# Kernel tuning notes

Measured on AMD Instinct MI355X. Metric: run time of the kernel, lower is better.

## Reference

```python
import jax, jax.numpy as jnp
import numpy as np

N, C, E, K = 50000, 128, 640000, 40  # nodes, feat dim, edges, classes
EPS = 1e-5


def setup_inputs() -> dict:
    key = jax.random.key(0)
    ks = jax.random.split(key, 8)
    s = 1.0 / np.sqrt(C)
    return {
        "x": jax.random.normal(ks[0], (N, C), jnp.float32),
        "edge_index": jax.random.randint(ks[1], (2, E), 0, N, dtype=jnp.int32),
        "W_conv": jax.random.normal(ks[2], (C, C), jnp.float32) * s,
        "b_conv": jnp.zeros((C,), jnp.float32),
        "gamma": jnp.ones((C,), jnp.float32),
        "beta": jnp.zeros((C,), jnp.float32),
        "W_fc": jax.random.normal(ks[3], (C, K), jnp.float32) * s,
        "b_fc": jnp.zeros((K,), jnp.float32),
    }


def reference(x, edge_index, W_conv, b_conv, gamma, beta, W_fc, b_fc):
    n = x.shape[0]
    loops = jnp.arange(n, dtype=edge_index.dtype)
    src = jnp.concatenate([edge_index[0], loops])  # add self-loops (PyG default)
    dst = jnp.concatenate([edge_index[1], loops])
    # symmetric normalization: deg^{-1/2}[src] * deg^{-1/2}[dst]
    deg = jax.ops.segment_sum(jnp.ones_like(dst, jnp.float32), dst, num_segments=n)
    dinv = jax.lax.rsqrt(jnp.maximum(deg, 1.0))  # deg >= 1 with self-loops
    norm = dinv[src] * dinv[dst]  # [E+N]
    h = x @ W_conv  # [N, C] transform before propagate (GCNConv)
    agg = jax.ops.segment_sum(h[src] * norm[:, None], dst, num_segments=n) + b_conv
    a = jax.nn.relu(agg) * x  # dropout = identity (eval mode); elementwise mul with residual
    mu = jnp.mean(a, axis=-1, keepdims=True)
    var = jnp.mean((a - mu) ** 2, axis=-1, keepdims=True)
    ln = (a - mu) * jax.lax.rsqrt(var + EPS) * gamma + beta
    return (ln + x) @ W_fc + b_fc
```

## Files before the change

kernel.cpp:

```cpp
#include <hip/hip_runtime.h>

#define C_DIM 128
#define EPS 1e-5f
#define DEG_CAP 64
#define NSCAT 625

typedef __attribute__((ext_vector_type(8))) short short8;
typedef __attribute__((ext_vector_type(4))) float f32x4;

__device__ __forceinline__ unsigned bf16rn(float f) {
    unsigned u = __float_as_uint(f);
    return (u + 0x7fffu + ((u >> 16) & 1u)) >> 16;
}
__device__ __forceinline__ unsigned pack_bf16(float lo, float hi) {
    return bf16rn(lo) | (bf16rn(hi) << 16);
}
__device__ __forceinline__ float blo(unsigned u) { return __uint_as_float(u << 16); }
__device__ __forceinline__ float bhi(unsigned u) { return __uint_as_float(u & 0xffff0000u); }

__global__ void prep(const float* __restrict__ Wc, const float* __restrict__ Wfc,
                     unsigned short* __restrict__ WcT, unsigned short* __restrict__ WT) {
    int tid = blockIdx.x * 256 + threadIdx.x;
    if (tid < 128 * 128) {
        int nc = tid >> 7, k = tid & 127;
        WcT[tid] = (unsigned short)bf16rn(Wc[k * C_DIM + nc]);
    } else if (tid < 128 * 128 + 48 * 128) {
        int t2 = tid - 128 * 128;
        int nc = t2 >> 7, k = t2 & 127;
        float v = (nc < 40) ? Wfc[k * 40 + nc] : 0.f;
        WT[t2] = (unsigned short)bf16rn(v);
    }
}

__global__ void fat(const float* __restrict__ x,
                    const unsigned short* __restrict__ WcT,
                    unsigned* __restrict__ hb,
                    const int* __restrict__ esrc,
                    const int* __restrict__ edst,
                    int* __restrict__ cnt16,
                    int* __restrict__ bsrc,
                    int n) {
    int b = blockIdx.x;
    int t = threadIdx.x;

    if (b < NSCAT) {
        const int S = NSCAT * 256;
        int i0 = b * 256 + t;
        int i1 = i0 + S, i2 = i1 + S, i3 = i2 + S;
        int d0 = edst[i0], d1 = edst[i1], d2 = edst[i2], d3 = edst[i3];
        int s0 = esrc[i0], s1 = esrc[i1], s2 = esrc[i2], s3 = esrc[i3];
        int p0 = atomicAdd(&cnt16[d0 * 16], 1);
        int p1 = atomicAdd(&cnt16[d1 * 16], 1);
        int p2 = atomicAdd(&cnt16[d2 * 16], 1);
        int p3 = atomicAdd(&cnt16[d3 * 16], 1);
        if (p0 < DEG_CAP) __builtin_nontemporal_store(s0, &bsrc[(long)d0 * DEG_CAP + p0]);
        if (p1 < DEG_CAP) __builtin_nontemporal_store(s1, &bsrc[(long)d1 * DEG_CAP + p1]);
        if (p2 < DEG_CAP) __builtin_nontemporal_store(s2, &bsrc[(long)d2 * DEG_CAP + p2]);
        if (p3 < DEG_CAP) __builtin_nontemporal_store(s3, &bsrc[(long)d3 * DEG_CAP + p3]);
    } else {
        int gb = b - NSCAT;
        int w = t >> 6, lane = t & 63;
        int rw = gb * 128 + w * 32;
        if (rw >= n) return;
        int mrow = lane & 15, quad = lane >> 4;
        f32x4 acc[2][8];
#pragma unroll
        for (int m = 0; m < 2; m++)
#pragma unroll
            for (int nt = 0; nt < 8; nt++) acc[m][nt] = (f32x4){0.f, 0.f, 0.f, 0.f};
        int r0 = rw + mrow;
        int r1 = rw + 16 + mrow;
        if (r0 >= n) r0 = n - 1;
        if (r1 >= n) r1 = n - 1;
#pragma unroll
        for (int ks = 0; ks < 4; ks++) {
            short8 A[2];
#pragma unroll
            for (int m = 0; m < 2; m++) {
                const float* px = &x[(long)(m ? r1 : r0) * C_DIM + ks * 32 + quad * 8];
                float4 xa = *(const float4*)px;
                float4 xb = *(const float4*)(px + 4);
                uint4 au;
                au.x = pack_bf16(xa.x, xa.y);
                au.y = pack_bf16(xa.z, xa.w);
                au.z = pack_bf16(xb.x, xb.y);
                au.w = pack_bf16(xb.z, xb.w);
                union { uint4 u; short8 s; } cv;
                cv.u = au;
                A[m] = cv.s;
            }
#pragma unroll
            for (int nt = 0; nt < 8; nt++) {
                short8 B = *(const short8*)&WcT[(nt * 16 + mrow) * 128 + ks * 32 + quad * 8];
                acc[0][nt] = __builtin_amdgcn_mfma_f32_16x16x32_bf16(A[0], B, acc[0][nt], 0, 0, 0);
                acc[1][nt] = __builtin_amdgcn_mfma_f32_16x16x32_bf16(A[1], B, acc[1][nt], 0, 0, 0);
            }
        }
        bool evenc = (mrow & 1) == 0;
#pragma unroll
        for (int m = 0; m < 2; m++)
#pragma unroll
            for (int nt = 0; nt < 8; nt++)
#pragma unroll
                for (int reg = 0; reg < 4; reg++) {
                    float v = acc[m][nt][reg];
                    float pv = __shfl_xor(v, 1);
                    int rr = rw + m * 16 + quad * 4 + reg;
                    if (evenc && rr < n)
                        hb[(long)rr * 64 + ((nt * 16 + mrow) >> 1)] = pack_bf16(v, pv);
                }
    }
}

__global__ void dinv_k(const int* __restrict__ cnt16, float* __restrict__ dinv, int n) {
    int i = blockIdx.x * blockDim.x + threadIdx.x;
    if (i < n) dinv[i] = rsqrtf((float)cnt16[i * 16] + 1.0f);
}

__global__ __launch_bounds__(256) void aggregate(const unsigned* __restrict__ hb,
                                                 const float* __restrict__ x,
                                                 const int* __restrict__ cnt16,
                                                 const int* __restrict__ bsrc,
                                                 const float* __restrict__ dinv,
                                                 const float* __restrict__ bconv,
                                                 const float* __restrict__ gamma,
                                                 const float* __restrict__ beta,
                                                 unsigned* __restrict__ zb, int n) {
    int wid = (blockIdx.x * blockDim.x + threadIdx.x) >> 6;
    if (wid >= n) return;
    int lane = threadIdx.x & 63;
    int sub = lane & 15, grp = lane >> 4;
    int i = wid;
    int degt = cnt16[i * 16];
    float di = dinv[i];
    int deg = degt > DEG_CAP ? DEG_CAP : degt;
    long base = (long)i * DEG_CAP;

    uint4 us = *(const uint4*)(hb + (long)i * 64 + sub * 4);
    float wself = (grp == 0) ? di * di : 0.f;
    float acc[8];
    acc[0] = wself * blo(us.x); acc[1] = wself * bhi(us.x);
    acc[2] = wself * blo(us.y); acc[3] = wself * bhi(us.y);
    acc[4] = wself * blo(us.z); acc[5] = wself * bhi(us.z);
    acc[6] = wself * blo(us.w); acc[7] = wself * bhi(us.w);

    int k = grp;
    for (; k + 4 < deg; k += 8) {
        int s0 = bsrc[base + k];
        int s1 = bsrc[base + k + 4];
        float w0 = dinv[s0] * di;
        float w1 = dinv[s1] * di;
        uint4 u0 = *(const uint4*)(hb + (long)s0 * 64 + sub * 4);
        uint4 u1 = *(const uint4*)(hb + (long)s1 * 64 + sub * 4);
        acc[0] += w0 * blo(u0.x); acc[1] += w0 * bhi(u0.x);
        acc[2] += w0 * blo(u0.y); acc[3] += w0 * bhi(u0.y);
        acc[4] += w0 * blo(u0.z); acc[5] += w0 * bhi(u0.z);
        acc[6] += w0 * blo(u0.w); acc[7] += w0 * bhi(u0.w);
        acc[0] += w1 * blo(u1.x); acc[1] += w1 * bhi(u1.x);
        acc[2] += w1 * blo(u1.y); acc[3] += w1 * bhi(u1.y);
        acc[4] += w1 * blo(u1.z); acc[5] += w1 * bhi(u1.z);
        acc[6] += w1 * blo(u1.w); acc[7] += w1 * bhi(u1.w);
    }
    for (; k < deg; k += 4) {
        int s = bsrc[base + k];
        float w = dinv[s] * di;
        uint4 u = *(const uint4*)(hb + (long)s * 64 + sub * 4);
        acc[0] += w * blo(u.x); acc[1] += w * bhi(u.x);
        acc[2] += w * blo(u.y); acc[3] += w * bhi(u.y);
        acc[4] += w * blo(u.z); acc[5] += w * bhi(u.z);
        acc[6] += w * blo(u.w); acc[7] += w * bhi(u.w);
    }

#pragma unroll
    for (int j = 0; j < 8; j++) {
        acc[j] += __shfl_xor(acc[j], 16);
        acc[j] += __shfl_xor(acc[j], 32);
    }

    float4 bca = *(const float4*)&bconv[sub * 8];
    float4 bcb = *(const float4*)&bconv[sub * 8 + 4];
    float4 xa  = *(const float4*)&x[(long)i * C_DIM + sub * 8];
    float4 xb  = *(const float4*)&x[(long)i * C_DIM + sub * 8 + 4];
    float a[8], xv[8];
    xv[0] = xa.x; xv[1] = xa.y; xv[2] = xa.z; xv[3] = xa.w;
    xv[4] = xb.x; xv[5] = xb.y; xv[6] = xb.z; xv[7] = xb.w;
    float bc[8] = {bca.x, bca.y, bca.z, bca.w, bcb.x, bcb.y, bcb.z, bcb.w};
#pragma unroll
    for (int j = 0; j < 8; j++) a[j] = fmaxf(acc[j] + bc[j], 0.f) * xv[j];

    float s = a[0] + a[1] + a[2] + a[3] + a[4] + a[5] + a[6] + a[7];
#pragma unroll
    for (int off = 1; off < 16; off <<= 1) s += __shfl_xor(s, off);
    float mu = s * (1.0f / 128.0f);
    float d[8], v = 0.f;
#pragma unroll
    for (int j = 0; j < 8; j++) { d[j] = a[j] - mu; v += d[j] * d[j]; }
#pragma unroll
    for (int off = 1; off < 16; off <<= 1) v += __shfl_xor(v, off);
    float inv = rsqrtf(v * (1.0f / 128.0f) + EPS);

    if (grp == 0) {
        float4 ga = *(const float4*)&gamma[sub * 8];
        float4 gb = *(const float4*)&gamma[sub * 8 + 4];
        float4 ba = *(const float4*)&beta[sub * 8];
        float4 bb = *(const float4*)&beta[sub * 8 + 4];
        float g[8] = {ga.x, ga.y, ga.z, ga.w, gb.x, gb.y, gb.z, gb.w};
        float be[8] = {ba.x, ba.y, ba.z, ba.w, bb.x, bb.y, bb.z, bb.w};
        float o[8];
#pragma unroll
        for (int j = 0; j < 8; j++) o[j] = d[j] * inv * g[j] + be[j] + xv[j];
        uint4 p;
        p.x = pack_bf16(o[0], o[1]);
        p.y = pack_bf16(o[2], o[3]);
        p.z = pack_bf16(o[4], o[5]);
        p.w = pack_bf16(o[6], o[7]);
        *(uint4*)(zb + (long)i * 64 + sub * 4) = p;
    }
}

__global__ __launch_bounds__(256) void gemm2(const unsigned short* __restrict__ zb,
                                             const unsigned short* __restrict__ WT,
                                             const float* __restrict__ bfc,
                                             float* __restrict__ out, int n) {
    int t = threadIdx.x;
    int w = t >> 6, lane = t & 63;
    int r0 = (blockIdx.x * 4 + w) * 64;
    if (r0 >= n) return;
    int mrow = lane & 15;
    int quad = lane >> 4;
    f32x4 acc[4][3];
#pragma unroll
    for (int m = 0; m < 4; m++)
#pragma unroll
        for (int nt = 0; nt < 3; nt++) acc[m][nt] = (f32x4){0.f, 0.f, 0.f, 0.f};
#pragma unroll
    for (int ks = 0; ks < 4; ks++) {
        short8 A[4], B[3];
#pragma unroll
        for (int m = 0; m < 4; m++) {
            int r = r0 + m * 16 + mrow;
            if (r >= n) r = n - 1;
            A[m] = *(const short8*)&zb[(long)r * 128 + ks * 32 + quad * 8];
        }
#pragma unroll
        for (int nt = 0; nt < 3; nt++)
            B[nt] = *(const short8*)&WT[(nt * 16 + mrow) * 128 + ks * 32 + quad * 8];
#pragma unroll
        for (int m = 0; m < 4; m++)
#pragma unroll
            for (int nt = 0; nt < 3; nt++)
                acc[m][nt] = __builtin_amdgcn_mfma_f32_16x16x32_bf16(A[m], B[nt], acc[m][nt], 0, 0, 0);
    }
#pragma unroll
    for (int nt = 0; nt < 3; nt++) {
        int c = nt * 16 + mrow;
        if (c < 40) {
            float bias = bfc[c];
#pragma unroll
            for (int m = 0; m < 4; m++) {
#pragma unroll
                for (int reg = 0; reg < 4; reg++) {
                    int r = r0 + m * 16 + quad * 4 + reg;
                    if (r < n) out[(long)r * 40 + c] = acc[m][nt][reg] + bias;
                }
            }
        }
    }
}

extern "C" void kernel_launch(void* const* d_in, const int* in_sizes, int n_in,
                              void* d_out, int out_size, void* d_ws, size_t ws_size,
                              hipStream_t stream) {
    const float* x     = (const float*)d_in[0];
    const int*   ei    = (const int*)d_in[1];
    const float* Wc    = (const float*)d_in[2];
    const float* bc    = (const float*)d_in[3];
    const float* gamma = (const float*)d_in[4];
    const float* beta  = (const float*)d_in[5];
    const float* Wfc   = (const float*)d_in[6];
    const float* bfc   = (const float*)d_in[7];
    float* out = (float*)d_out;

    int N = in_sizes[0] / C_DIM;
    int E = in_sizes[1] / 2;
    const int* esrc = ei;
    const int* edst = ei + E;
    (void)E;

    char* p = (char*)d_ws;
    auto carve = [&](size_t bytes) {
        void* q = (void*)p;
        p += (bytes + 255) & ~(size_t)255;
        return q;
    };
    unsigned* hb        = (unsigned*)carve((size_t)N * 64 * 4);
    unsigned* zb        = (unsigned*)carve((size_t)N * 64 * 4);
    unsigned short* WcT = (unsigned short*)carve(128 * 128 * 2);
    unsigned short* WT  = (unsigned short*)carve(48 * 128 * 2);
    float* dinv         = (float*)carve((size_t)N * 4);
    int*   cnt16        = (int*)carve((size_t)N * 64);
    int*   bsrc         = (int*)carve((size_t)N * DEG_CAP * 4);

    (void)hipMemsetAsync(cnt16, 0, (size_t)N * 64, stream);

    prep<<<(128 * 128 + 48 * 128 + 255) / 256, 256, 0, stream>>>(Wc, Wfc, WcT, WT);

    int g1 = (N + 127) / 128;
    fat<<<NSCAT + g1, 256, 0, stream>>>(x, WcT, hb, esrc, edst, cnt16, bsrc, N);

    dinv_k<<<(N + 255) / 256, 256, 0, stream>>>(cnt16, dinv, N);

    aggregate<<<((size_t)N * 64 + 255) / 256, 256, 0, stream>>>(
        hb, x, cnt16, bsrc, dinv, bc, gamma, beta, zb, N);

    gemm2<<<(N / 64 + 4) / 4, 256, 0, stream>>>((const unsigned short*)zb, WT, bfc, out, N);
}
```

Before: 185.6 us.

## Build CSR by two-level bucket sort instead of global atomic padded lists

Replaces the per-destination global atomic counters and fixed-capacity padded neighbor lists with a two-pass radix-style sort: a per-block shared-memory histogram over 128-node buckets, a single-block scan, a scatter into bucket-sorted packed (dst,src) pairs, and a per-bucket kernel that builds an exact CSR rowptr/bsrc and dinv. This removes the contended global atomics, the memset and the degree cap, and gives the aggregate kernel contiguous neighbor ranges. In exchange it adds more launches, a serial single-block scan, and an extra round trip through an 8-byte sorted array.

Result: slower. 268.8 us (+44.8%).

```diff
diff --git a/kernel.cpp b/kernel.cpp
--- a/kernel.cpp
+++ b/kernel.cpp
@@ -2,8 +2,8 @@
 
 #define C_DIM 128
 #define EPS 1e-5f
-#define DEG_CAP 64
-#define NSCAT 625
+#define NHB 160
+#define MAXNB 512
 
 typedef __attribute__((ext_vector_type(8))) short short8;
 typedef __attribute__((ext_vector_type(4))) float f32x4;
@@ -18,47 +18,76 @@
 __device__ __forceinline__ float blo(unsigned u) { return __uint_as_float(u << 16); }
 __device__ __forceinline__ float bhi(unsigned u) { return __uint_as_float(u & 0xffff0000u); }
 
-__global__ void prep(const float* __restrict__ Wc, const float* __restrict__ Wfc,
-                     unsigned short* __restrict__ WcT, unsigned short* __restrict__ WT) {
-    int tid = blockIdx.x * 256 + threadIdx.x;
-    if (tid < 128 * 128) {
-        int nc = tid >> 7, k = tid & 127;
-        WcT[tid] = (unsigned short)bf16rn(Wc[k * C_DIM + nc]);
-    } else if (tid < 128 * 128 + 48 * 128) {
-        int t2 = tid - 128 * 128;
-        int nc = t2 >> 7, k = t2 & 127;
-        float v = (nc < 40) ? Wfc[k * 40 + nc] : 0.f;
-        WT[t2] = (unsigned short)bf16rn(v);
-    }
-}
-
-__global__ void fat(const float* __restrict__ x,
-                    const unsigned short* __restrict__ WcT,
-                    unsigned* __restrict__ hb,
-                    const int* __restrict__ esrc,
-                    const int* __restrict__ edst,
-                    int* __restrict__ cnt16,
-                    int* __restrict__ bsrc,
-                    int n) {
-    int b = blockIdx.x;
+__global__ __launch_bounds__(256) void k_hist(const int* __restrict__ edst,
+                                              int* __restrict__ gh, int nb, int e, int epb,
+                                              const float* __restrict__ Wc,
+                                              const float* __restrict__ Wfc,
+                                              unsigned short* __restrict__ WcT,
+                                              unsigned short* __restrict__ WT) {
+    int b = blockIdx.x, t = threadIdx.x;
+    if (b < NHB) {
+        __shared__ int hist[MAXNB];
+        for (int i = t; i < nb; i += 256) hist[i] = 0;
+        __syncthreads();
+        int base = b * epb;
+        int end = min(e, base + epb);
+        for (int i = base + t; i < end; i += 256)
+            atomicAdd(&hist[edst[i] >> 7], 1);
+        __syncthreads();
+        for (int i = t; i < nb; i += 256) gh[i * NHB + b] = hist[i];
+    } else {
+        for (int tid = t; tid < 128 * 128; tid += 256) {
+            int nc = tid >> 7, k = tid & 127;
+            WcT[tid] = (unsigned short)bf16rn(Wc[k * C_DIM + nc]);
+        }
+        for (int tid = t; tid < 48 * 128; tid += 256) {
+            int nc = tid >> 7, k = tid & 127;
+            float v = (nc < 40) ? Wfc[k * 40 + nc] : 0.f;
+            WT[tid] = (unsigned short)bf16rn(v);
+        }
+    }
+}
+
+__global__ __launch_bounds__(1024) void k_scan(int* __restrict__ gh, int len) {
+    __shared__ int ts[1024];
     int t = threadIdx.x;
-
-    if (b < NSCAT) {
-        const int S = NSCAT * 256;
-        int i0 = b * 256 + t;
-        int i1 = i0 + S, i2 = i1 + S, i3 = i2 + S;
-        int d0 = edst[i0], d1 = edst[i1], d2 = edst[i2], d3 = edst[i3];
-        int s0 = esrc[i0], s1 = esrc[i1], s2 = esrc[i2], s3 = esrc[i3];
-        int p0 = atomicAdd(&cnt16[d0 * 16], 1);
-        int p1 = atomicAdd(&cnt16[d1 * 16], 1);
-        int p2 = atomicAdd(&cnt16[d2 * 16], 1);
-        int p3 = atomicAdd(&cnt16[d3 * 16], 1);
-        if (p0 < DEG_CAP) __builtin_nontemporal_store(s0, &bsrc[(long)d0 * DEG_CAP + p0]);
-        if (p1 < DEG_CAP) __builtin_nontemporal_store(s1, &bsrc[(long)d1 * DEG_CAP + p1]);
-        if (p2 < DEG_CAP) __builtin_nontemporal_store(s2, &bsrc[(long)d2 * DEG_CAP + p2]);
-        if (p3 < DEG_CAP) __builtin_nontemporal_store(s3, &bsrc[(long)d3 * DEG_CAP + p3]);
+    int c = (len + 1023) >> 10;
+    int lo = t * c, hi = min(len, lo + c);
+    int s = 0;
+    for (int i = lo; i < hi; i++) s += gh[i];
+    ts[t] = s;
+    __syncthreads();
+    for (int off = 1; off < 1024; off <<= 1) {
+        int v = (t >= off) ? ts[t - off] : 0;
+        __syncthreads();
+        ts[t] += v;
+        __syncthreads();
+    }
+    int run = (t > 0) ? ts[t - 1] : 0;
+    for (int i = lo; i < hi; i++) { int v = gh[i]; gh[i] = run; run += v; }
+}
+
+__global__ __launch_bounds__(256) void k_fat(const int* __restrict__ esrc,
+                                             const int* __restrict__ edst,
+                                             const int* __restrict__ gh,
+                                             long long* __restrict__ sorted,
+                                             const float* __restrict__ x,
+                                             const unsigned short* __restrict__ WcT,
+                                             unsigned* __restrict__ hb,
+                                             int nb, int e, int epb, int n) {
+    int b = blockIdx.x, t = threadIdx.x;
+    if (b < NHB) {
+        __shared__ int cur[MAXNB];
+        for (int i = t; i < nb; i += 256) cur[i] = gh[i * NHB + b];
+        __syncthreads();
+        int base = b * epb, end = min(e, base + epb);
+        for (int i = base + t; i < end; i += 256) {
+            int d = edst[i], s = esrc[i];
+            int pos = atomicAdd(&cur[d >> 7], 1);
+            sorted[pos] = (((long long)d) << 32) | (unsigned int)s;
+        }
     } else {
-        int gb = b - NSCAT;
+        int gb = b - NHB;
         int w = t >> 6, lane = t & 63;
         int rw = gb * 128 + w * 32;
         if (rw >= n) return;
@@ -112,14 +141,51 @@
     }
 }
 
-__global__ void dinv_k(const int* __restrict__ cnt16, float* __restrict__ dinv, int n) {
-    int i = blockIdx.x * blockDim.x + threadIdx.x;
-    if (i < n) dinv[i] = rsqrtf((float)cnt16[i * 16] + 1.0f);
+__global__ __launch_bounds__(256) void k_csr(const long long* __restrict__ sorted,
+                                             const int* __restrict__ gh,
+                                             int* __restrict__ bsrc,
+                                             int* __restrict__ rowptr,
+                                             float* __restrict__ dinv,
+                                             int nb, int n, int e) {
+    __shared__ int h[128], basep[128], cur[128];
+    int b = blockIdx.x, t = threadIdx.x;
+    int node0 = b << 7;
+    int nloc = min(128, n - node0);
+    int start = gh[b * NHB];
+    int end = (b + 1 < nb) ? gh[(b + 1) * NHB] : e;
+    if (t < 128) h[t] = 0;
+    __syncthreads();
+    for (int i = start + t; i < end; i += 256)
+        atomicAdd(&h[(int)(sorted[i] >> 32) & 127], 1);
+    __syncthreads();
+    if (t < 128) basep[t] = h[t];
+    __syncthreads();
+    for (int off = 1; off < 128; off <<= 1) {
+        int v = 0;
+        if (t < 128 && t >= off) v = basep[t - off];
+        __syncthreads();
+        if (t < 128) basep[t] += v;
+        __syncthreads();
+    }
+    int excl = (t < 128) ? (basep[t] - h[t]) : 0;
+    if (t < nloc) {
+        rowptr[node0 + t] = start + excl;
+        dinv[node0 + t] = rsqrtf((float)h[t] + 1.0f);
+    }
+    if (b == nb - 1 && t == 0) rowptr[n] = e;
+    if (t < 128) cur[t] = excl;
+    __syncthreads();
+    for (int i = start + t; i < end; i += 256) {
+        long long pk = sorted[i];
+        int dl = (int)(pk >> 32) & 127;
+        int pos = atomicAdd(&cur[dl], 1);
+        bsrc[start + pos] = (int)(pk & 0xffffffffLL);
+    }
 }
 
 __global__ __launch_bounds__(256) void aggregate(const unsigned* __restrict__ hb,
                                                  const float* __restrict__ x,
-                                                 const int* __restrict__ cnt16,
+                                                 const int* __restrict__ rowptr,
                                                  const int* __restrict__ bsrc,
                                                  const float* __restrict__ dinv,
                                                  const float* __restrict__ bconv,
@@ -131,10 +197,8 @@
     int lane = threadIdx.x & 63;
     int sub = lane & 15, grp = lane >> 4;
     int i = wid;
-    int degt = cnt16[i * 16];
     float di = dinv[i];
-    int deg = degt > DEG_CAP ? DEG_CAP : degt;
-    long base = (long)i * DEG_CAP;
+    int beg = rowptr[i], end = rowptr[i + 1];
 
     uint4 us = *(const uint4*)(hb + (long)i * 64 + sub * 4);
     float wself = (grp == 0) ? di * di : 0.f;
@@ -144,10 +208,10 @@
     acc[4] = wself * blo(us.z); acc[5] = wself * bhi(us.z);
     acc[6] = wself * blo(us.w); acc[7] = wself * bhi(us.w);
 
-    int k = grp;
-    for (; k + 4 < deg; k += 8) {
-        int s0 = bsrc[base + k];
-        int s1 = bsrc[base + k + 4];
+    int k = beg + grp;
+    for (; k + 4 < end; k += 8) {
+        int s0 = bsrc[k];
+        int s1 = bsrc[k + 4];
         float w0 = dinv[s0] * di;
         float w1 = dinv[s1] * di;
         uint4 u0 = *(const uint4*)(hb + (long)s0 * 64 + sub * 4);
@@ -161,8 +225,8 @@
         acc[4] += w1 * blo(u1.z); acc[5] += w1 * bhi(u1.z);
         acc[6] += w1 * blo(u1.w); acc[7] += w1 * bhi(u1.w);
     }
-    for (; k < deg; k += 4) {
-        int s = bsrc[base + k];
+    for (; k < end; k += 4) {
+        int s = bsrc[k];
         float w = dinv[s] * di;
         uint4 u = *(const uint4*)(hb + (long)s * 64 + sub * 4);
         acc[0] += w * blo(u.x); acc[1] += w * bhi(u.x);
@@ -285,7 +349,9 @@
     int E = in_sizes[1] / 2;
     const int* esrc = ei;
     const int* edst = ei + E;
-    (void)E;
+
+    int nb  = (N + 127) >> 7;
+    int epb = (E + NHB - 1) / NHB;
 
     char* p = (char*)d_ws;
     auto carve = [&](size_t bytes) {
@@ -298,20 +364,19 @@
     unsigned short* WcT = (unsigned short*)carve(128 * 128 * 2);
     unsigned short* WT  = (unsigned short*)carve(48 * 128 * 2);
     float* dinv         = (float*)carve((size_t)N * 4);
-    int*   cnt16        = (int*)carve((size_t)N * 64);
-    int*   bsrc         = (int*)carve((size_t)N * DEG_CAP * 4);
-
-    (void)hipMemsetAsync(cnt16, 0, (size_t)N * 64, stream);
-
-    prep<<<(128 * 128 + 48 * 128 + 255) / 256, 256, 0, stream>>>(Wc, Wfc, WcT, WT);
-
+    int*   gh           = (int*)carve((size_t)nb * NHB * 4);
+    long long* sorted   = (long long*)carve((size_t)E * 8);
+    int*   bsrc         = (int*)carve((size_t)E * 4);
+    int*   rowptr       = (int*)carve((size_t)(N + 1) * 4);
+
+    k_hist<<<NHB + 1, 256, 0, stream>>>(edst, gh, nb, E, epb, Wc, Wfc, WcT, WT);
+    k_scan<<<1, 1024, 0, stream>>>(gh, nb * NHB);
     int g1 = (N + 127) / 128;
-    fat<<<NSCAT + g1, 256, 0, stream>>>(x, WcT, hb, esrc, edst, cnt16, bsrc, N);
-
-    dinv_k<<<(N + 255) / 256, 256, 0, stream>>>(cnt16, dinv, N);
+    k_fat<<<NHB + g1, 256, 0, stream>>>(esrc, edst, gh, sorted, x, WcT, hb, nb, E, epb, N);
+    k_csr<<<nb, 256, 0, stream>>>(sorted, gh, bsrc, rowptr, dinv, nb, N, E);
 
     aggregate<<<((size_t)N * 64 + 255) / 256, 256, 0, stream>>>(
-        hb, x, cnt16, bsrc, dinv, bc, gamma, beta, zb, N);
+        hb, x, rowptr, bsrc, dinv, bc, gamma, beta, zb, N);
 
     gemm2<<<(N / 64 + 4) / 4, 256, 0, stream>>>((const unsigned short*)zb, WT, bfc, out, N);
 }
```
